# Performance work log

Measured on AMD Instinct MI355X. Metric: run time of the kernel, lower is better.

## Reference

```python
import jax, jax.numpy as jnp
import numpy as np

N = 100000
E = 1600000
F1 = 512
F3 = 128
H = 128
C = 64
SW = 0.2
FW = 1.0 - SW
BN_EPS = 1e-5


def setup_inputs() -> dict:
    key = jax.random.key(0)
    ks = jax.random.split(key, 12)
    def glorot(k, shape):
        lim = float(np.sqrt(6.0 / (shape[0] + shape[1])))
        return jax.random.uniform(k, shape, jnp.float32, -lim, lim)
    return {
        "x1": jax.random.normal(ks[0], (N, F1), jnp.float32),
        "x2": jax.random.normal(ks[1], (N, F3), jnp.float32),
        "edge_index": jax.random.randint(ks[2], (2, E), 0, N, jnp.int64),
        "W1": glorot(ks[3], (F1, H)), "b1": jnp.zeros((H,), jnp.float32),
        "W2": glorot(ks[4], (F3, H)), "b2": jnp.zeros((H,), jnp.float32),
        "Wg1": glorot(ks[5], (H, H)), "bg1": jnp.zeros((H,), jnp.float32),
        "Wg2": glorot(ks[6], (H, C)), "bg2": jnp.zeros((C,), jnp.float32),
        "gamma": jnp.ones((H,), jnp.float32), "beta": jnp.zeros((H,), jnp.float32),
        "rmean": jnp.zeros((H,), jnp.float32), "rvar": jnp.ones((H,), jnp.float32),
    }


def reference(x1, x2, edge_index, W1, b1, W2, b2, Wg1, bg1, Wg2, bg2, gamma, beta, rmean, rvar):
    # Embedding blend: fw * lin1(features) + sw * lin2(structural embedding)
    h = FW * (x1 @ W1 + b1) + SW * (x2 @ W2 + b2)  # [N, H]
    src, dst = edge_index[0], edge_index[1]
    # GCNConv layer 1 (normalize=False, add_self_loops=False): transform then scatter-add
    z = h @ Wg1                                              # [N, H]
    agg = jax.ops.segment_sum(z[src], dst, num_segments=N) + bg1  # [N, H]
    # BatchNorm1d (eval, running stats) + ReLU; dropout is identity in eval
    agg = (agg - rmean) * jax.lax.rsqrt(rvar + BN_EPS) * gamma + beta
    agg = jax.nn.relu(agg)
    # GCNConv layer 2 -> logits
    z2 = agg @ Wg2                                           # [N, C]
    out = jax.ops.segment_sum(z2[src], dst, num_segments=N) + bg2
    return out
```

## Files before the change

### kernel.cpp

```cpp
#include <hip/hip_runtime.h>
#include <hip/hip_fp16.h>
#include <cstddef>

#define NN    100000
#define EE    1600000
#define F1D   512
#define F3D   128
#define HD    128
#define CD    64
#define SWc   0.2f
#define FWc   0.8f
#define BN_EPS 1e-5f

#define SCAN_B 1024
#define NB ((NN + SCAN_B - 1) / SCAN_B)

#define BSH   7
#define NBKA  1024
#define NBUK  ((NN + 127) / 128)
#define CHK   4096
#define BCAP  8192

typedef _Float16 half8 __attribute__((ext_vector_type(8)));
typedef float f32x4 __attribute__((ext_vector_type(4)));

__global__ __launch_bounds__(256) void count_kernel(
    const int* __restrict__ dst, int* __restrict__ deg)
{
    int e = blockIdx.x * 256 + threadIdx.x;
    if (e < EE) atomicAdd(&deg[dst[e]], 1);
}

__global__ __launch_bounds__(SCAN_B) void scan_partial_kernel(
    const int* __restrict__ deg, int* __restrict__ partials)
{
    __shared__ int sh[SCAN_B / 64];
    int i = blockIdx.x * SCAN_B + threadIdx.x;
    int v = (i < NN) ? deg[i] : 0;
#pragma unroll
    for (int d = 32; d > 0; d >>= 1) v += __shfl_down(v, d, 64);
    int lane = threadIdx.x & 63, wv = threadIdx.x >> 6;
    if (lane == 0) sh[wv] = v;
    __syncthreads();
    if (threadIdx.x < SCAN_B / 64) {
        int s = sh[threadIdx.x];
#pragma unroll
        for (int d = SCAN_B / 128; d > 0; d >>= 1) s += __shfl_down(s, d, 64);
        if (threadIdx.x == 0) partials[blockIdx.x] = s;
    }
}

__global__ __launch_bounds__(128) void scan_base_kernel(
    int* __restrict__ partials, int* __restrict__ offsets)
{
    __shared__ int sh[128];
    int t = threadIdx.x;
    int v = (t < NB) ? partials[t] : 0;
    sh[t] = v;
    __syncthreads();
    for (int d = 1; d < 128; d <<= 1) {
        int u = (t >= d) ? sh[t - d] : 0;
        __syncthreads();
        sh[t] += u;
        __syncthreads();
    }
    if (t < NB) partials[t] = sh[t] - v;
    if (t == NB - 1) offsets[NN] = sh[t];
}

__global__ __launch_bounds__(SCAN_B) void scan_apply_kernel(
    const int* __restrict__ deg, const int* __restrict__ partials,
    int* __restrict__ offsets, int* __restrict__ cursor)
{
    __shared__ int sh[SCAN_B];
    int t = threadIdx.x;
    int i = blockIdx.x * SCAN_B + t;
    int v = (i < NN) ? deg[i] : 0;
    sh[t] = v;
    __syncthreads();
    for (int d = 1; d < SCAN_B; d <<= 1) {
        int u = (t >= d) ? sh[t - d] : 0;
        __syncthreads();
        sh[t] += u;
        __syncthreads();
    }
    if (i < NN) {
        int excl = sh[t] - v + partials[blockIdx.x];
        offsets[i] = excl;
        cursor[i]  = excl;
    }
}

__global__ __launch_bounds__(256) void binit_kernel(
    const int* __restrict__ offsets, int* __restrict__ gcur)
{
    int b = blockIdx.x * 256 + threadIdx.x;
    if (b < NBKA) {
        int n = b << BSH;
        if (n > NN) n = NN;
        gcur[b] = offsets[n];
    }
}

__global__ __launch_bounds__(256) void bucket_kernel(
    const int* __restrict__ src, const int* __restrict__ dst,
    int* __restrict__ gcur, int* __restrict__ ebuf)
{
    __shared__ int hist[NBKA];
    __shared__ int gb2[NBKA];
    __shared__ int tsum[256];
    __shared__ int stage[CHK];
    __shared__ int destg[CHK];

    const int t  = threadIdx.x;
    const int e0 = blockIdx.x * CHK;
    int ecnt = EE - e0;
    if (ecnt > CHK) ecnt = CHK;

    for (int b = t; b < NBKA; b += 256) hist[b] = 0;
    __syncthreads();

    for (int i = t; i < ecnt; i += 256) {
        int d = dst[e0 + i];
        atomicAdd(&hist[d >> BSH], 1);
    }
    __syncthreads();

    int a0 = hist[4 * t], a1 = hist[4 * t + 1];
    int a2 = hist[4 * t + 2], a3 = hist[4 * t + 3];
    int tot = a0 + a1 + a2 + a3;
    tsum[t] = tot;
    __syncthreads();
    for (int d = 1; d < 256; d <<= 1) {
        int u = (t >= d) ? tsum[t - d] : 0;
        __syncthreads();
        tsum[t] += u;
        __syncthreads();
    }
    int base = tsum[t] - tot;
    int o0 = base, o1 = base + a0, o2 = base + a0 + a1, o3 = base + a0 + a1 + a2;
    if (a0 > 0) gb2[4 * t]     = atomicAdd(&gcur[4 * t],     a0) - o0;
    if (a1 > 0) gb2[4 * t + 1] = atomicAdd(&gcur[4 * t + 1], a1) - o1;
    if (a2 > 0) gb2[4 * t + 2] = atomicAdd(&gcur[4 * t + 2], a2) - o2;
    if (a3 > 0) gb2[4 * t + 3] = atomicAdd(&gcur[4 * t + 3], a3) - o3;
    hist[4 * t] = o0; hist[4 * t + 1] = o1;
    hist[4 * t + 2] = o2; hist[4 * t + 3] = o3;
    __syncthreads();

    for (int i = t; i < ecnt; i += 256) {
        int d = dst[e0 + i];
        int s = src[e0 + i];
        int b = d >> BSH;
        int pos = atomicAdd(&hist[b], 1);
        stage[pos] = (s << BSH) | (d & 127);
        destg[pos] = gb2[b] + pos;
    }
    __syncthreads();

    for (int sx = t; sx < ecnt; sx += 256) ebuf[destg[sx]] = stage[sx];
}

__global__ __launch_bounds__(256) void csr_place_kernel(
    const int* __restrict__ ebuf, const int* __restrict__ offsets,
    int* __restrict__ cursor, int* __restrict__ csr)
{
    __shared__ int lcur[128];
    __shared__ int stage[BCAP];

    const int b   = blockIdx.x;
    const int t   = threadIdx.x;
    const int nb0 = b << BSH;
    int nb1 = nb0 + 128;
    if (nb1 > NN) nb1 = NN;
    const int rbeg = offsets[nb0];
    const int rend = offsets[nb1];
    const int L = rend - rbeg;

    if (L <= BCAP) {
        if (t < nb1 - nb0) lcur[t] = offsets[nb0 + t] - rbeg;
        __syncthreads();
        for (int e = rbeg + t; e < rend; e += 256) {
            int p = ebuf[e];
            int pos = atomicAdd(&lcur[p & 127], 1);
            stage[pos] = p >> BSH;
        }
        __syncthreads();
        for (int s = t; s < L; s += 256) csr[rbeg + s] = stage[s];
    } else {
        for (int e = rbeg + t; e < rend; e += 256) {
            int p = ebuf[e];
            int node = nb0 + (p & 127);
            int pos = atomicAdd(&cursor[node], 1);
            csr[pos] = p >> BSH;
        }
    }
}

__global__ __launch_bounds__(256) void prep_kernel(
    const float* __restrict__ W1, const float* __restrict__ W2,
    const float* __restrict__ Wg1, const float* __restrict__ Wg2,
    const float* __restrict__ b1, const float* __restrict__ b2,
    _Float16* __restrict__ Wc_t, _Float16* __restrict__ Wg1_t,
    _Float16* __restrict__ Wg2_t, float* __restrict__ hbuf)
{
    int i = blockIdx.x * 256 + threadIdx.x;
    if (i < 128 * 640) {
        int n = i / 640, k = i % 640;
        float v = (k < F1D) ? FWc * W1[(size_t)k * HD + n]
                            : SWc * W2[(size_t)(k - F1D) * HD + n];
        Wc_t[i] = (_Float16)v;
    } else if (i < 128 * 640 + 128 * 128) {
        int j = i - 128 * 640; int n = j / 128, k = j % 128;
        Wg1_t[j] = (_Float16)Wg1[(size_t)k * HD + n];
    } else if (i < 128 * 640 + 128 * 128 + 64 * 128) {
        int j = i - 128 * 640 - 128 * 128; int n = j / 128, k = j % 128;
        Wg2_t[j] = (_Float16)Wg2[(size_t)k * CD + n];
    } else if (i < 128 * 640 + 128 * 128 + 64 * 128 + 128) {
        int j = i - (128 * 640 + 128 * 128 + 64 * 128);
        hbuf[j] = FWc * b1[j] + SWc * b2[j];
    }
}

__global__ __launch_bounds__(256) void gemm1_mfma(
    const float* __restrict__ x1, const float* __restrict__ x2,
    const _Float16* __restrict__ Wc_t, const _Float16* __restrict__ Wg1_t,
    const float* __restrict__ hbuf, _Float16* __restrict__ z)
{
    __shared__ __align__(16) _Float16 As[128][72];
    __shared__ __align__(16) _Float16 Bs[128][72];
    __shared__ __align__(16) _Float16 Hs[128][136];

    const int tid  = threadIdx.x;
    const int wave = tid >> 6;
    const int lane = tid & 63;
    const int quad = lane >> 4;
    const int l16  = lane & 15;
    const int row0 = blockIdx.x * 128;

    const int sr = tid >> 1;
    const int sc = (tid & 1) * 32;

    f32x4 acc[2][8];
    const f32x4 zero4 = {0.f, 0.f, 0.f, 0.f};
#pragma unroll
    for (int mi = 0; mi < 2; ++mi)
#pragma unroll
        for (int ni = 0; ni < 8; ++ni) acc[mi][ni] = zero4;

    for (int t = 0; t < 10; ++t) {
        const float* xp; int stride, kb;
        if (t < 8) { xp = x1; stride = F1D; kb = t * 64; }
        else       { xp = x2; stride = F3D; kb = (t - 8) * 64; }
        __syncthreads();
        {
            int gr = row0 + sr;
            if (gr < NN) {
                const float4* rp = (const float4*)(xp + (size_t)gr * stride + kb + sc);
#pragma unroll
                for (int i = 0; i < 4; ++i) {
                    float4 f0 = rp[2 * i];
                    float4 f1 = rp[2 * i + 1];
                    half8 hv = { (_Float16)f0.x, (_Float16)f0.y, (_Float16)f0.z, (_Float16)f0.w,
                                 (_Float16)f1.x, (_Float16)f1.y, (_Float16)f1.z, (_Float16)f1.w };
                    *(half8*)&As[sr][sc + i * 8] = hv;
                }
            } else {
                half8 zv = { (_Float16)0.f, (_Float16)0.f, (_Float16)0.f, (_Float16)0.f,
                             (_Float16)0.f, (_Float16)0.f, (_Float16)0.f, (_Float16)0.f };
#pragma unroll
                for (int i = 0; i < 4; ++i) *(half8*)&As[sr][sc + i * 8] = zv;
            }
            const _Float16* wp = Wc_t + (size_t)sr * 640 + t * 64 + sc;
#pragma unroll
            for (int i = 0; i < 4; ++i)
                *(half8*)&Bs[sr][sc + i * 8] = *(const half8*)(wp + i * 8);
        }
        __syncthreads();
#pragma unroll
        for (int ks = 0; ks < 2; ++ks) {
            half8 a[2], b[8];
#pragma unroll
            for (int mi = 0; mi < 2; ++mi)
                a[mi] = *(const half8*)&As[wave * 32 + mi * 16 + l16][ks * 32 + quad * 8];
#pragma unroll
            for (int ni = 0; ni < 8; ++ni)
                b[ni] = *(const half8*)&Bs[ni * 16 + l16][ks * 32 + quad * 8];
#pragma unroll
            for (int mi = 0; mi < 2; ++mi)
#pragma unroll
                for (int ni = 0; ni < 8; ++ni)
                    acc[mi][ni] = __builtin_amdgcn_mfma_f32_16x16x32_f16(
                        a[mi], b[ni], acc[mi][ni], 0, 0, 0);
        }
    }

    {
        float hbv[8];
#pragma unroll
        for (int ni = 0; ni < 8; ++ni) hbv[ni] = hbuf[ni * 16 + l16];
#pragma unroll
        for (int mi = 0; mi < 2; ++mi)
#pragma unroll
            for (int ni = 0; ni < 8; ++ni)
#pragma unroll
                for (int r = 0; r < 4; ++r)
                    Hs[wave * 32 + mi * 16 + quad * 4 + r][ni * 16 + l16] =
                        (_Float16)(acc[mi][ni][r] + hbv[ni]);
    }

#pragma unroll
    for (int mi = 0; mi < 2; ++mi)
#pragma unroll
        for (int ni = 0; ni < 8; ++ni) acc[mi][ni] = zero4;

    for (int t = 0; t < 2; ++t) {
        __syncthreads();
        {
            const _Float16* wp = Wg1_t + (size_t)sr * 128 + t * 64 + sc;
#pragma unroll
            for (int i = 0; i < 4; ++i)
                *(half8*)&Bs[sr][sc + i * 8] = *(const half8*)(wp + i * 8);
        }
        __syncthreads();
#pragma unroll
        for (int ks = 0; ks < 2; ++ks) {
            half8 a[2], b[8];
#pragma unroll
            for (int mi = 0; mi < 2; ++mi)
                a[mi] = *(const half8*)&Hs[wave * 32 + mi * 16 + l16][t * 64 + ks * 32 + quad * 8];
#pragma unroll
            for (int ni = 0; ni < 8; ++ni)
                b[ni] = *(const half8*)&Bs[ni * 16 + l16][ks * 32 + quad * 8];
#pragma unroll
            for (int mi = 0; mi < 2; ++mi)
#pragma unroll
                for (int ni = 0; ni < 8; ++ni)
                    acc[mi][ni] = __builtin_amdgcn_mfma_f32_16x16x32_f16(
                        a[mi], b[ni], acc[mi][ni], 0, 0, 0);
        }
    }

#pragma unroll
    for (int mi = 0; mi < 2; ++mi)
#pragma unroll
        for (int ni = 0; ni < 8; ++ni)
#pragma unroll
            for (int r = 0; r < 4; ++r)
                Hs[wave * 32 + mi * 16 + quad * 4 + r][ni * 16 + l16] =
                    (_Float16)acc[mi][ni][r];
    __syncthreads();
    {
        int gr = row0 + sr;
        if (gr < NN) {
            int c0 = (tid & 1) * 64;
            _Float16* zp = z + (size_t)gr * HD + c0;
#pragma unroll
            for (int i = 0; i < 8; ++i)
                *(half8*)(zp + i * 8) = *(const half8*)&Hs[sr][c0 + i * 8];
        }
    }
}

__global__ __launch_bounds__(256) void gemm2_mfma(
    const float* __restrict__ agg, const _Float16* __restrict__ Wg2_t,
    const float* __restrict__ bg1, const float* __restrict__ gamma,
    const float* __restrict__ beta, const float* __restrict__ rmean,
    const float* __restrict__ rvar, _Float16* __restrict__ z2)
{
    __shared__ __align__(16) _Float16 As[128][72];
    __shared__ __align__(16) _Float16 Bs[64][72];
    __shared__ float sS[HD], sT[HD];

    const int tid = threadIdx.x;
    if (tid < HD) {
        float s = gamma[tid] * rsqrtf(rvar[tid] + BN_EPS);
        sS[tid] = s;
        sT[tid] = (bg1[tid] - rmean[tid]) * s + beta[tid];
    }
    __syncthreads();

    const int wave = tid >> 6;
    const int lane = tid & 63;
    const int quad = lane >> 4;
    const int l16  = lane & 15;
    const int row0 = blockIdx.x * 128;
    const int sr = tid >> 1;
    const int sc = (tid & 1) * 32;

    f32x4 acc[2][4];
    const f32x4 zero4 = {0.f, 0.f, 0.f, 0.f};
#pragma unroll
    for (int mi = 0; mi < 2; ++mi)
#pragma unroll
        for (int ni = 0; ni < 4; ++ni) acc[mi][ni] = zero4;

    for (int t = 0; t < 2; ++t) {
        __syncthreads();
        {
            int gr = row0 + sr;
            if (gr < NN) {
                const float4* rp = (const float4*)(agg + (size_t)gr * HD + t * 64 + sc);
#pragma unroll
                for (int i = 0; i < 4; ++i) {
                    float4 f0 = rp[2 * i];
                    float4 f1 = rp[2 * i + 1];
                    int k = t * 64 + sc + i * 8;
                    float v0 = fmaxf(fmaf(f0.x, sS[k + 0], sT[k + 0]), 0.f);
                    float v1 = fmaxf(fmaf(f0.y, sS[k + 1], sT[k + 1]), 0.f);
                    float v2 = fmaxf(fmaf(f0.z, sS[k + 2], sT[k + 2]), 0.f);
                    float v3 = fmaxf(fmaf(f0.w, sS[k + 3], sT[k + 3]), 0.f);
                    float v4 = fmaxf(fmaf(f1.x, sS[k + 4], sT[k + 4]), 0.f);
                    float v5 = fmaxf(fmaf(f1.y, sS[k + 5], sT[k + 5]), 0.f);
                    float v6 = fmaxf(fmaf(f1.z, sS[k + 6], sT[k + 6]), 0.f);
                    float v7 = fmaxf(fmaf(f1.w, sS[k + 7], sT[k + 7]), 0.f);
                    half8 hv = { (_Float16)v0, (_Float16)v1, (_Float16)v2, (_Float16)v3,
                                 (_Float16)v4, (_Float16)v5, (_Float16)v6, (_Float16)v7 };
                    *(half8*)&As[sr][sc + i * 8] = hv;
                }
            } else {
                half8 zv = { (_Float16)0.f, (_Float16)0.f, (_Float16)0.f, (_Float16)0.f,
                             (_Float16)0.f, (_Float16)0.f, (_Float16)0.f, (_Float16)0.f };
#pragma unroll
                for (int i = 0; i < 4; ++i) *(half8*)&As[sr][sc + i * 8] = zv;
            }
            int n = tid >> 2, c = (tid & 3) * 16;
            const _Float16* wp = Wg2_t + (size_t)n * 128 + t * 64 + c;
            *(half8*)&Bs[n][c]     = *(const half8*)wp;
            *(half8*)&Bs[n][c + 8] = *(const half8*)(wp + 8);
        }
        __syncthreads();
#pragma unroll
        for (int ks = 0; ks < 2; ++ks) {
            half8 a[2], b[4];
#pragma unroll
            for (int mi = 0; mi < 2; ++mi)
                a[mi] = *(const half8*)&As[wave * 32 + mi * 16 + l16][ks * 32 + quad * 8];
#pragma unroll
            for (int ni = 0; ni < 4; ++ni)
                b[ni] = *(const half8*)&Bs[ni * 16 + l16][ks * 32 + quad * 8];
#pragma unroll
            for (int mi = 0; mi < 2; ++mi)
#pragma unroll
                for (int ni = 0; ni < 4; ++ni)
                    acc[mi][ni] = __builtin_amdgcn_mfma_f32_16x16x32_f16(
                        a[mi], b[ni], acc[mi][ni], 0, 0, 0);
        }
    }

    __syncthreads();
#pragma unroll
    for (int mi = 0; mi < 2; ++mi)
#pragma unroll
        for (int ni = 0; ni < 4; ++ni)
#pragma unroll
            for (int r = 0; r < 4; ++r)
                As[wave * 32 + mi * 16 + quad * 4 + r][ni * 16 + l16] =
                    (_Float16)acc[mi][ni][r];
    __syncthreads();
    {
        int gr = row0 + sr;
        if (gr < NN) {
            _Float16* zp = z2 + (size_t)gr * CD + sc;
            *(half8*)(zp)      = *(const half8*)&As[sr][sc];
            *(half8*)(zp + 8)  = *(const half8*)&As[sr][sc + 8];
            *(half8*)(zp + 16) = *(const half8*)&As[sr][sc + 16];
            *(half8*)(zp + 24) = *(const half8*)&As[sr][sc + 24];
        }
    }
}

__global__ __launch_bounds__(256) void gather1_kernel(
    const _Float16* __restrict__ z, const int* __restrict__ offsets,
    const int* __restrict__ csr_src, float* __restrict__ agg)
{
    int node = blockIdx.x * 4 + (threadIdx.x >> 6);
    if (node >= NN) return;
    const int lane = threadIdx.x & 63;
    const int h  = lane >> 4;
    const int fl = lane & 15;

    int beg = offsets[node];
    int cnt = offsets[node + 1] - beg;

    float a0 = 0.f, a1 = 0.f, a2 = 0.f, a3 = 0.f;
    float a4 = 0.f, a5 = 0.f, a6 = 0.f, a7 = 0.f;

    for (int j0 = 0; j0 < cnt; j0 += 64) {
        int cntc = cnt - j0; if (cntc > 64) cntc = 64;
        int myidx = (lane < cntc) ? csr_src[beg + j0 + lane] : 0;
        int nq = (cntc + 3) >> 2;
#pragma unroll 4
        for (int i = 0; i < nq; ++i) {
            int e = i * 4 + h;
            int si = __shfl(myidx, e);
            float m = (e < cntc) ? 1.f : 0.f;
            float4 raw = *(const float4*)(z + (size_t)si * HD + fl * 8);
            const __half2* hp = (const __half2*)&raw;
            float2 f0 = __half22float2(hp[0]);
            float2 f1 = __half22float2(hp[1]);
            float2 f2 = __half22float2(hp[2]);
            float2 f3 = __half22float2(hp[3]);
            a0 = fmaf(m, f0.x, a0); a1 = fmaf(m, f0.y, a1);
            a2 = fmaf(m, f1.x, a2); a3 = fmaf(m, f1.y, a3);
            a4 = fmaf(m, f2.x, a4); a5 = fmaf(m, f2.y, a5);
            a6 = fmaf(m, f3.x, a6); a7 = fmaf(m, f3.y, a7);
        }
    }

    a0 += __shfl_xor(a0, 16); a1 += __shfl_xor(a1, 16);
    a2 += __shfl_xor(a2, 16); a3 += __shfl_xor(a3, 16);
    a4 += __shfl_xor(a4, 16); a5 += __shfl_xor(a5, 16);
    a6 += __shfl_xor(a6, 16); a7 += __shfl_xor(a7, 16);
    a0 += __shfl_xor(a0, 32); a1 += __shfl_xor(a1, 32);
    a2 += __shfl_xor(a2, 32); a3 += __shfl_xor(a3, 32);
    a4 += __shfl_xor(a4, 32); a5 += __shfl_xor(a5, 32);
    a6 += __shfl_xor(a6, 32); a7 += __shfl_xor(a7, 32);

    if (h == 0) {
        float* op = agg + (size_t)node * HD + fl * 8;
        float4 o0 = make_float4(a0, a1, a2, a3);
        float4 o1 = make_float4(a4, a5, a6, a7);
        *(float4*)op       = o0;
        *(float4*)(op + 4) = o1;
    }
}

__global__ __launch_bounds__(256) void gather2_kernel(
    const _Float16* __restrict__ z2, const int* __restrict__ offsets,
    const int* __restrict__ csr_src, const float* __restrict__ bg2,
    float* __restrict__ out)
{
    int node = blockIdx.x * 4 + (threadIdx.x >> 6);
    if (node >= NN) return;
    const int lane = threadIdx.x & 63;
    const int h  = lane >> 4;
    const int fl = lane & 15;

    int beg = offsets[node];
    int cnt = offsets[node + 1] - beg;

    float a0 = 0.f, a1 = 0.f, a2 = 0.f, a3 = 0.f;

    for (int j0 = 0; j0 < cnt; j0 += 64) {
        int cntc = cnt - j0; if (cntc > 64) cntc = 64;
        int myidx = (lane < cntc) ? csr_src[beg + j0 + lane] : 0;
        int nq = (cntc + 3) >> 2;
#pragma unroll 4
        for (int i = 0; i < nq; ++i) {
            int e = i * 4 + h;
            int si = __shfl(myidx, e);
            float m = (e < cntc) ? 1.f : 0.f;
            float2 raw = *(const float2*)(z2 + (size_t)si * CD + fl * 4);
            const __half2* hp = (const __half2*)&raw;
            float2 f0 = __half22float2(hp[0]);
            float2 f1 = __half22float2(hp[1]);
            a0 = fmaf(m, f0.x, a0); a1 = fmaf(m, f0.y, a1);
            a2 = fmaf(m, f1.x, a2); a3 = fmaf(m, f1.y, a3);
        }
    }

    a0 += __shfl_xor(a0, 16); a1 += __shfl_xor(a1, 16);
    a2 += __shfl_xor(a2, 16); a3 += __shfl_xor(a3, 16);
    a0 += __shfl_xor(a0, 32); a1 += __shfl_xor(a1, 32);
    a2 += __shfl_xor(a2, 32); a3 += __shfl_xor(a3, 32);

    if (h == 0) {
        float4 bv = *(const float4*)(bg2 + fl * 4);
        float4 o = make_float4(a0 + bv.x, a1 + bv.y, a2 + bv.z, a3 + bv.w);
        *(float4*)(out + (size_t)node * CD + fl * 4) = o;
    }
}

extern "C" void kernel_launch(void* const* d_in, const int* in_sizes, int n_in,
                              void* d_out, int out_size, void* d_ws, size_t ws_size,
                              hipStream_t stream)
{
    const float* x1    = (const float*)d_in[0];
    const float* x2    = (const float*)d_in[1];
    const int*   ei    = (const int*)d_in[2];
    const float* W1    = (const float*)d_in[3];
    const float* b1    = (const float*)d_in[4];
    const float* W2    = (const float*)d_in[5];
    const float* b2    = (const float*)d_in[6];
    const float* Wg1   = (const float*)d_in[7];
    const float* bg1   = (const float*)d_in[8];
    const float* Wg2   = (const float*)d_in[9];
    const float* bg2   = (const float*)d_in[10];
    const float* gamma = (const float*)d_in[11];
    const float* beta  = (const float*)d_in[12];
    const float* rmean = (const float*)d_in[13];
    const float* rvar  = (const float*)d_in[14];
    float* out = (float*)d_out;

    char* p = (char*)d_ws;
    _Float16* z_h  = (_Float16*)p; p += (size_t)NN * HD * sizeof(_Float16);
    float*  agg    = (float*)p;    p += (size_t)NN * HD * sizeof(float);
    int*    csr    = (int*)p;      p += (size_t)EE * sizeof(int);
    int*    offs   = (int*)p;      p += (size_t)(NN + 16) * sizeof(int);
    int*    curs   = (int*)p;      p += (size_t)(NN + 16) * sizeof(int);
    int*    deg    = (int*)p;      p += (size_t)(NN + 16) * sizeof(int);
    int*    parts  = (int*)p;      p += (size_t)(NB + 16) * sizeof(int);
    int*    gcur   = (int*)p;      p += (size_t)(NBKA + 16) * sizeof(int);
    _Float16* Wc_t = (_Float16*)p; p += (size_t)128 * 640 * sizeof(_Float16);
    _Float16* Wg1t = (_Float16*)p; p += (size_t)128 * 128 * sizeof(_Float16);
    _Float16* Wg2t = (_Float16*)p; p += (size_t)64 * 128 * sizeof(_Float16);
    float*  hbuf   = (float*)p;    p += 128 * sizeof(float);
    _Float16* z2_h = z_h;
    int*    ebuf   = (int*)agg;

    const int* src = ei;
    const int* dst = ei + EE;

    prep_kernel<<<(128 * 640 + 128 * 128 + 64 * 128 + 128 + 255) / 256, 256, 0, stream>>>(
        W1, W2, Wg1, Wg2, b1, b2, Wc_t, Wg1t, Wg2t, hbuf);

    hipMemsetAsync(deg, 0, (size_t)NN * sizeof(int), stream);
    count_kernel<<<(EE + 255) / 256, 256, 0, stream>>>(dst, deg);
    scan_partial_kernel<<<NB, SCAN_B, 0, stream>>>(deg, parts);
    scan_base_kernel<<<1, 128, 0, stream>>>(parts, offs);
    scan_apply_kernel<<<NB, SCAN_B, 0, stream>>>(deg, parts, offs, curs);
    binit_kernel<<<(NBKA + 255) / 256, 256, 0, stream>>>(offs, gcur);
    bucket_kernel<<<(EE + CHK - 1) / CHK, 256, 0, stream>>>(src, dst, gcur, ebuf);
    csr_place_kernel<<<NBUK, 256, 0, stream>>>(ebuf, offs, curs, csr);

    gemm1_mfma<<<(NN + 127) / 128, 256, 0, stream>>>(x1, x2, Wc_t, Wg1t, hbuf, z_h);
    gather1_kernel<<<(NN + 3) / 4, 256, 0, stream>>>(z_h, offs, csr, agg);
    gemm2_mfma<<<(NN + 127) / 128, 256, 0, stream>>>(agg, Wg2t, bg1, gamma, beta,
                                                     rmean, rvar, z2_h);
    gather2_kernel<<<(NN + 3) / 4, 256, 0, stream>>>(z2_h, offs, csr, bg2, out);
}
```

Measured before the change: 641.2 us.

## Prefetch next gemm1 K-tile into registers and alias LDS buffers for occupancy

gemm1 now loads the next K-tile of x and the fused weights into registers while MFMAs run on the current LDS tile, so global load latency overlaps with compute. The LDS arrays are packed into one dynamic pool in which Hs aliases As/Bs, and the second GEMM gets its own Bs2 region. Launch bounds request 3 blocks per CU. The register prefetch raises VGPR pressure, and the occupancy hint may force spills.

```diff
diff --git a/kernel.cpp b/kernel.cpp
--- a/kernel.cpp
+++ b/kernel.cpp
@@ -20,6 +20,8 @@
 #define NBUK  ((NN + 127) / 128)
 #define CHK   4096
 #define BCAP  8192
+
+#define G1_LDS 53248
 
 typedef _Float16 half8 __attribute__((ext_vector_type(8)));
 typedef float f32x4 __attribute__((ext_vector_type(4)));
@@ -221,14 +223,16 @@
     }
 }
 
-__global__ __launch_bounds__(256) void gemm1_mfma(
+__global__ __launch_bounds__(256, 3) void gemm1_mfma(
     const float* __restrict__ x1, const float* __restrict__ x2,
     const _Float16* __restrict__ Wc_t, const _Float16* __restrict__ Wg1_t,
     const float* __restrict__ hbuf, _Float16* __restrict__ z)
 {
-    __shared__ __align__(16) _Float16 As[128][72];
-    __shared__ __align__(16) _Float16 Bs[128][72];
-    __shared__ __align__(16) _Float16 Hs[128][136];
+    extern __shared__ char pool[];
+    _Float16 (*As)[72]  = (_Float16(*)[72])pool;
+    _Float16 (*Bs)[72]  = (_Float16(*)[72])(pool + 18432);
+    _Float16 (*Hs)[136] = (_Float16(*)[136])pool;
+    _Float16 (*Bs2)[72] = (_Float16(*)[72])(pool + 34816);
 
     const int tid  = threadIdx.x;
     const int wave = tid >> 6;
@@ -239,6 +243,8 @@
 
     const int sr = tid >> 1;
     const int sc = (tid & 1) * 32;
+    const int gr = row0 + sr;
+    const bool valid = gr < NN;
 
     f32x4 acc[2][8];
     const f32x4 zero4 = {0.f, 0.f, 0.f, 0.f};
@@ -247,35 +253,56 @@
 #pragma unroll
         for (int ni = 0; ni < 8; ++ni) acc[mi][ni] = zero4;
 
+    float4 xr[8];
+    half8  wr[4];
+
+    {
+        if (valid) {
+            const float4* rp = (const float4*)(x1 + (size_t)gr * F1D + sc);
+#pragma unroll
+            for (int i = 0; i < 8; ++i) xr[i] = rp[i];
+        }
+        const _Float16* wp = Wc_t + (size_t)sr * 640 + sc;
+#pragma unroll
+        for (int i = 0; i < 4; ++i) wr[i] = *(const half8*)(wp + i * 8);
+    }
+
     for (int t = 0; t < 10; ++t) {
-        const float* xp; int stride, kb;
-        if (t < 8) { xp = x1; stride = F1D; kb = t * 64; }
-        else       { xp = x2; stride = F3D; kb = (t - 8) * 64; }
-        __syncthreads();
-        {
-            int gr = row0 + sr;
-            if (gr < NN) {
+        if (valid) {
+#pragma unroll
+            for (int i = 0; i < 4; ++i) {
+                float4 f0 = xr[2 * i];
+                float4 f1 = xr[2 * i + 1];
+                half8 hv = { (_Float16)f0.x, (_Float16)f0.y, (_Float16)f0.z, (_Float16)f0.w,
+                             (_Float16)f1.x, (_Float16)f1.y, (_Float16)f1.z, (_Float16)f1.w };
+                *(half8*)&As[sr][sc + i * 8] = hv;
+            }
+        } else {
+            half8 zv = { (_Float16)0.f, (_Float16)0.f, (_Float16)0.f, (_Float16)0.f,
+                         (_Float16)0.f, (_Float16)0.f, (_Float16)0.f, (_Float16)0.f };
+#pragma unroll
+            for (int i = 0; i < 4; ++i) *(half8*)&As[sr][sc + i * 8] = zv;
+        }
+#pragma unroll
+        for (int i = 0; i < 4; ++i)
+            *(half8*)&Bs[sr][sc + i * 8] = wr[i];
+
+        __syncthreads();
+
+        if (t + 1 < 10) {
+            const float* xp; int stride, kb;
+            if (t + 1 < 8) { xp = x1; stride = F1D; kb = (t + 1) * 64; }
+            else           { xp = x2; stride = F3D; kb = (t + 1 - 8) * 64; }
+            if (valid) {
                 const float4* rp = (const float4*)(xp + (size_t)gr * stride + kb + sc);
 #pragma unroll
-                for (int i = 0; i < 4; ++i) {
-                    float4 f0 = rp[2 * i];
-                    float4 f1 = rp[2 * i + 1];
-                    half8 hv = { (_Float16)f0.x, (_Float16)f0.y, (_Float16)f0.z, (_Float16)f0.w,
-                                 (_Float16)f1.x, (_Float16)f1.y, (_Float16)f1.z, (_Float16)f1.w };
-                    *(half8*)&As[sr][sc + i * 8] = hv;
-                }
-            } else {
-                half8 zv = { (_Float16)0.f, (_Float16)0.f, (_Float16)0.f, (_Float16)0.f,
-                             (_Float16)0.f, (_Float16)0.f, (_Float16)0.f, (_Float16)0.f };
-#pragma unroll
-                for (int i = 0; i < 4; ++i) *(half8*)&As[sr][sc + i * 8] = zv;
+                for (int i = 0; i < 8; ++i) xr[i] = rp[i];
             }
-            const _Float16* wp = Wc_t + (size_t)sr * 640 + t * 64 + sc;
-#pragma unroll
-            for (int i = 0; i < 4; ++i)
-                *(half8*)&Bs[sr][sc + i * 8] = *(const half8*)(wp + i * 8);
-        }
-        __syncthreads();
+            const _Float16* wp = Wc_t + (size_t)sr * 640 + (t + 1) * 64 + sc;
+#pragma unroll
+            for (int i = 0; i < 4; ++i) wr[i] = *(const half8*)(wp + i * 8);
+        }
+
 #pragma unroll
         for (int ks = 0; ks < 2; ++ks) {
             half8 a[2], b[8];
@@ -292,6 +319,7 @@
                     acc[mi][ni] = __builtin_amdgcn_mfma_f32_16x16x32_f16(
                         a[mi], b[ni], acc[mi][ni], 0, 0, 0);
         }
+        __syncthreads();
     }
 
     {
@@ -319,7 +347,7 @@
             const _Float16* wp = Wg1_t + (size_t)sr * 128 + t * 64 + sc;
 #pragma unroll
             for (int i = 0; i < 4; ++i)
-                *(half8*)&Bs[sr][sc + i * 8] = *(const half8*)(wp + i * 8);
+                *(half8*)&Bs2[sr][sc + i * 8] = *(const half8*)(wp + i * 8);
         }
         __syncthreads();
 #pragma unroll
@@ -330,7 +358,7 @@
                 a[mi] = *(const half8*)&Hs[wave * 32 + mi * 16 + l16][t * 64 + ks * 32 + quad * 8];
 #pragma unroll
             for (int ni = 0; ni < 8; ++ni)
-                b[ni] = *(const half8*)&Bs[ni * 16 + l16][ks * 32 + quad * 8];
+                b[ni] = *(const half8*)&Bs2[ni * 16 + l16][ks * 32 + quad * 8];
 #pragma unroll
             for (int mi = 0; mi < 2; ++mi)
 #pragma unroll
@@ -350,8 +378,7 @@
                     (_Float16)acc[mi][ni][r];
     __syncthreads();
     {
-        int gr = row0 + sr;
-        if (gr < NN) {
+        if (valid) {
             int c0 = (tid & 1) * 64;
             _Float16* zp = z + (size_t)gr * HD + c0;
 #pragma unroll
@@ -623,7 +650,7 @@
     bucket_kernel<<<(EE + CHK - 1) / CHK, 256, 0, stream>>>(src, dst, gcur, ebuf);
     csr_place_kernel<<<NBUK, 256, 0, stream>>>(ebuf, offs, curs, csr);
 
-    gemm1_mfma<<<(NN + 127) / 128, 256, 0, stream>>>(x1, x2, Wc_t, Wg1t, hbuf, z_h);
+    gemm1_mfma<<<(NN + 127) / 128, 256, G1_LDS, stream>>>(x1, x2, Wc_t, Wg1t, hbuf, z_h);
     gather1_kernel<<<(NN + 3) / 4, 256, 0, stream>>>(z_h, offs, csr, agg);
     gemm2_mfma<<<(NN + 127) / 128, 256, 0, stream>>>(agg, Wg2t, bg1, gamma, beta,
                                                      rmean, rvar, z2_h);
```

New measurement: 638.4 us. About the same (-0.4%).

## Fold Wg1 into the blended embedding weights and retile gemm1

Applied to the files above, without the earlier changes.

A new prep kernel precomputes the fused weight (FW*W1 ; SW*W2) @ Wg1 and the fused bias, so gemm1 runs a single 640x128 GEMM instead of a GEMM followed by a second 128x128 GEMM and an intermediate fp16 store of h. gemm1 now uses 64-row tiles with larger K chunks (256) and fewer barriers, and reads B fragments straight from global/L2 instead of staging them in LDS. It also sets launch bounds for 4 blocks per CU. The costs are that B loads are no longer shared through LDS, and the fused product is rounded to fp16 once, which changes numerics slightly.

```diff
diff --git a/kernel.cpp b/kernel.cpp
--- a/kernel.cpp
+++ b/kernel.cpp
@@ -197,166 +197,151 @@
 }
 
 __global__ __launch_bounds__(256) void prep_kernel(
+    const float* __restrict__ Wg2, const float* __restrict__ b1,
+    const float* __restrict__ b2, _Float16* __restrict__ Wg2_t,
+    float* __restrict__ hbuf)
+{
+    int i = blockIdx.x * 256 + threadIdx.x;
+    if (i < 64 * 128) {
+        int n = i / 128, k = i % 128;
+        Wg2_t[i] = (_Float16)Wg2[(size_t)k * CD + n];
+    } else if (i < 64 * 128 + 128) {
+        int j = i - 64 * 128;
+        hbuf[j] = FWc * b1[j] + SWc * b2[j];
+    }
+}
+
+__global__ __launch_bounds__(128) void prep_fuse_kernel(
     const float* __restrict__ W1, const float* __restrict__ W2,
-    const float* __restrict__ Wg1, const float* __restrict__ Wg2,
-    const float* __restrict__ b1, const float* __restrict__ b2,
-    _Float16* __restrict__ Wc_t, _Float16* __restrict__ Wg1_t,
-    _Float16* __restrict__ Wg2_t, float* __restrict__ hbuf)
-{
-    int i = blockIdx.x * 256 + threadIdx.x;
-    if (i < 128 * 640) {
-        int n = i / 640, k = i % 640;
-        float v = (k < F1D) ? FWc * W1[(size_t)k * HD + n]
+    const float* __restrict__ Wg1, const float* __restrict__ hbuf,
+    _Float16* __restrict__ Wf_t, float* __restrict__ bz)
+{
+    __shared__ float wrow[128];
+    const int k = blockIdx.x;
+    const int n = threadIdx.x;
+    if (k < 640) {
+        wrow[n] = (k < F1D) ? FWc * W1[(size_t)k * HD + n]
                             : SWc * W2[(size_t)(k - F1D) * HD + n];
-        Wc_t[i] = (_Float16)v;
-    } else if (i < 128 * 640 + 128 * 128) {
-        int j = i - 128 * 640; int n = j / 128, k = j % 128;
-        Wg1_t[j] = (_Float16)Wg1[(size_t)k * HD + n];
-    } else if (i < 128 * 640 + 128 * 128 + 64 * 128) {
-        int j = i - 128 * 640 - 128 * 128; int n = j / 128, k = j % 128;
-        Wg2_t[j] = (_Float16)Wg2[(size_t)k * CD + n];
-    } else if (i < 128 * 640 + 128 * 128 + 64 * 128 + 128) {
-        int j = i - (128 * 640 + 128 * 128 + 64 * 128);
-        hbuf[j] = FWc * b1[j] + SWc * b2[j];
-    }
-}
-
-__global__ __launch_bounds__(256) void gemm1_mfma(
+        __syncthreads();
+        float acc = 0.f;
+#pragma unroll 8
+        for (int j = 0; j < 128; ++j)
+            acc = fmaf(wrow[j], Wg1[(size_t)j * HD + n], acc);
+        Wf_t[(size_t)n * 640 + k] = (_Float16)acc;
+    } else {
+        wrow[n] = hbuf[n];
+        __syncthreads();
+        float acc = 0.f;
+#pragma unroll 8
+        for (int j = 0; j < 128; ++j)
+            acc = fmaf(wrow[j], Wg1[(size_t)j * HD + n], acc);
+        bz[n] = acc;
+    }
+}
+
+__global__ __launch_bounds__(256, 4) void gemm1_mfma(
     const float* __restrict__ x1, const float* __restrict__ x2,
-    const _Float16* __restrict__ Wc_t, const _Float16* __restrict__ Wg1_t,
-    const float* __restrict__ hbuf, _Float16* __restrict__ z)
-{
-    __shared__ __align__(16) _Float16 As[128][72];
-    __shared__ __align__(16) _Float16 Bs[128][72];
-    __shared__ __align__(16) _Float16 Hs[128][136];
+    const _Float16* __restrict__ Wf_t, const float* __restrict__ bz,
+    _Float16* __restrict__ z)
+{
+    __shared__ __align__(16) _Float16 As[64][264];
 
     const int tid  = threadIdx.x;
     const int wave = tid >> 6;
     const int lane = tid & 63;
     const int quad = lane >> 4;
     const int l16  = lane & 15;
-    const int row0 = blockIdx.x * 128;
-
-    const int sr = tid >> 1;
-    const int sc = (tid & 1) * 32;
-
-    f32x4 acc[2][8];
+    const int row0 = blockIdx.x * 64;
+
+    const int sr = tid >> 2;
+    const int sq = tid & 3;
+    const int gr = row0 + sr;
+    const bool valid = gr < NN;
+
+    f32x4 acc[4][2];
     const f32x4 zero4 = {0.f, 0.f, 0.f, 0.f};
 #pragma unroll
-    for (int mi = 0; mi < 2; ++mi)
-#pragma unroll
-        for (int ni = 0; ni < 8; ++ni) acc[mi][ni] = zero4;
-
-    for (int t = 0; t < 10; ++t) {
-        const float* xp; int stride, kb;
-        if (t < 8) { xp = x1; stride = F1D; kb = t * 64; }
-        else       { xp = x2; stride = F3D; kb = (t - 8) * 64; }
+    for (int mi = 0; mi < 4; ++mi)
+#pragma unroll
+        for (int ni = 0; ni < 2; ++ni) acc[mi][ni] = zero4;
+
+#pragma unroll
+    for (int s = 0; s < 3; ++s) {
+        const int kbW = s * 256;
+        const int BKs = (s < 2) ? 256 : 128;
+        const float* xp = (s < 2) ? (x1 + (size_t)gr * F1D + s * 256)
+                                  : (x2 + (size_t)gr * F3D);
+        const int scf = sq * (BKs >> 2);
         __syncthreads();
         {
-            int gr = row0 + sr;
-            if (gr < NN) {
-                const float4* rp = (const float4*)(xp + (size_t)gr * stride + kb + sc);
-#pragma unroll
-                for (int i = 0; i < 4; ++i) {
-                    float4 f0 = rp[2 * i];
-                    float4 f1 = rp[2 * i + 1];
-                    half8 hv = { (_Float16)f0.x, (_Float16)f0.y, (_Float16)f0.z, (_Float16)f0.w,
+            const int nf4 = BKs >> 4;
+            if (valid) {
+                const float4* rp = (const float4*)(xp + scf);
+#pragma unroll
+                for (int c = 0; c < nf4; c += 4) {
+                    float4 f0 = rp[c], f1 = rp[c + 1];
+                    float4 f2 = rp[c + 2], f3 = rp[c + 3];
+                    half8 h0 = { (_Float16)f0.x, (_Float16)f0.y, (_Float16)f0.z, (_Float16)f0.w,
                                  (_Float16)f1.x, (_Float16)f1.y, (_Float16)f1.z, (_Float16)f1.w };
-                    *(half8*)&As[sr][sc + i * 8] = hv;
+                    half8 h1 = { (_Float16)f2.x, (_Float16)f2.y, (_Float16)f2.z, (_Float16)f2.w,
+                                 (_Float16)f3.x, (_Float16)f3.y, (_Float16)f3.z, (_Float16)f3.w };
+                    *(half8*)&As[sr][scf + c * 4]     = h0;
+                    *(half8*)&As[sr][scf + c * 4 + 8] = h1;
                 }
             } else {
                 half8 zv = { (_Float16)0.f, (_Float16)0.f, (_Float16)0.f, (_Float16)0.f,
                              (_Float16)0.f, (_Float16)0.f, (_Float16)0.f, (_Float16)0.f };
 #pragma unroll
-                for (int i = 0; i < 4; ++i) *(half8*)&As[sr][sc + i * 8] = zv;
+                for (int c = 0; c < nf4; c += 4) {
+                    *(half8*)&As[sr][scf + c * 4]     = zv;
+                    *(half8*)&As[sr][scf + c * 4 + 8] = zv;
+                }
             }
-            const _Float16* wp = Wc_t + (size_t)sr * 640 + t * 64 + sc;
-#pragma unroll
-            for (int i = 0; i < 4; ++i)
-                *(half8*)&Bs[sr][sc + i * 8] = *(const half8*)(wp + i * 8);
-        }
-        __syncthreads();
-#pragma unroll
-        for (int ks = 0; ks < 2; ++ks) {
-            half8 a[2], b[8];
-#pragma unroll
-            for (int mi = 0; mi < 2; ++mi)
-                a[mi] = *(const half8*)&As[wave * 32 + mi * 16 + l16][ks * 32 + quad * 8];
-#pragma unroll
-            for (int ni = 0; ni < 8; ++ni)
-                b[ni] = *(const half8*)&Bs[ni * 16 + l16][ks * 32 + quad * 8];
-#pragma unroll
-            for (int mi = 0; mi < 2; ++mi)
-#pragma unroll
-                for (int ni = 0; ni < 8; ++ni)
+        }
+        __syncthreads();
+
+        const int nks = BKs >> 5;
+        const _Float16* bbase = Wf_t + (size_t)(wave * 32 + l16) * 640 + kbW + quad * 8;
+#pragma unroll
+        for (int ks = 0; ks < nks; ++ks) {
+            half8 a[4], b[2];
+#pragma unroll
+            for (int mi = 0; mi < 4; ++mi)
+                a[mi] = *(const half8*)&As[mi * 16 + l16][ks * 32 + quad * 8];
+            b[0] = *(const half8*)(bbase + ks * 32);
+            b[1] = *(const half8*)(bbase + 16 * 640 + ks * 32);
+#pragma unroll
+            for (int mi = 0; mi < 4; ++mi)
+#pragma unroll
+                for (int ni = 0; ni < 2; ++ni)
                     acc[mi][ni] = __builtin_amdgcn_mfma_f32_16x16x32_f16(
                         a[mi], b[ni], acc[mi][ni], 0, 0, 0);
         }
     }
 
+    __syncthreads();
     {
-        float hbv[8];
-#pragma unroll
-        for (int ni = 0; ni < 8; ++ni) hbv[ni] = hbuf[ni * 16 + l16];
-#pragma unroll
-        for (int mi = 0; mi < 2; ++mi)
-#pragma unroll
-            for (int ni = 0; ni < 8; ++ni)
+        float bzv[2];
+        bzv[0] = bz[wave * 32 + l16];
+        bzv[1] = bz[wave * 32 + 16 + l16];
+#pragma unroll
+        for (int mi = 0; mi < 4; ++mi)
+#pragma unroll
+            for (int ni = 0; ni < 2; ++ni)
 #pragma unroll
                 for (int r = 0; r < 4; ++r)
-                    Hs[wave * 32 + mi * 16 + quad * 4 + r][ni * 16 + l16] =
-                        (_Float16)(acc[mi][ni][r] + hbv[ni]);
-    }
-
-#pragma unroll
-    for (int mi = 0; mi < 2; ++mi)
-#pragma unroll
-        for (int ni = 0; ni < 8; ++ni) acc[mi][ni] = zero4;
-
-    for (int t = 0; t < 2; ++t) {
-        __syncthreads();
-        {
-            const _Float16* wp = Wg1_t + (size_t)sr * 128 + t * 64 + sc;
+                    As[mi * 16 + quad * 4 + r][wave * 32 + ni * 16 + l16] =
+                        (_Float16)(acc[mi][ni][r] + bzv[ni]);
+    }
+    __syncthreads();
+    {
+        int zr = tid >> 2;
+        int c0 = (tid & 3) * 32;
+        if (row0 + zr < NN) {
+            _Float16* zp = z + (size_t)(row0 + zr) * HD + c0;
 #pragma unroll
             for (int i = 0; i < 4; ++i)
-                *(half8*)&Bs[sr][sc + i * 8] = *(const half8*)(wp + i * 8);
-        }
-        __syncthreads();
-#pragma unroll
-        for (int ks = 0; ks < 2; ++ks) {
-            half8 a[2], b[8];
-#pragma unroll
-            for (int mi = 0; mi < 2; ++mi)
-                a[mi] = *(const half8*)&Hs[wave * 32 + mi * 16 + l16][t * 64 + ks * 32 + quad * 8];
-#pragma unroll
-            for (int ni = 0; ni < 8; ++ni)
-                b[ni] = *(const half8*)&Bs[ni * 16 + l16][ks * 32 + quad * 8];
-#pragma unroll
-            for (int mi = 0; mi < 2; ++mi)
-#pragma unroll
-                for (int ni = 0; ni < 8; ++ni)
-                    acc[mi][ni] = __builtin_amdgcn_mfma_f32_16x16x32_f16(
-                        a[mi], b[ni], acc[mi][ni], 0, 0, 0);
-        }
-    }
-
-#pragma unroll
-    for (int mi = 0; mi < 2; ++mi)
-#pragma unroll
-        for (int ni = 0; ni < 8; ++ni)
-#pragma unroll
-            for (int r = 0; r < 4; ++r)
-                Hs[wave * 32 + mi * 16 + quad * 4 + r][ni * 16 + l16] =
-                    (_Float16)acc[mi][ni][r];
-    __syncthreads();
-    {
-        int gr = row0 + sr;
-        if (gr < NN) {
-            int c0 = (tid & 1) * 64;
-            _Float16* zp = z + (size_t)gr * HD + c0;
-#pragma unroll
-            for (int i = 0; i < 8; ++i)
-                *(half8*)(zp + i * 8) = *(const half8*)&Hs[sr][c0 + i * 8];
+                *(half8*)(zp + i * 8) = *(const half8*)&As[zr][c0 + i * 8];
         }
     }
 }
@@ -601,9 +586,9 @@
     int*    deg    = (int*)p;      p += (size_t)(NN + 16) * sizeof(int);
     int*    parts  = (int*)p;      p += (size_t)(NB + 16) * sizeof(int);
     int*    gcur   = (int*)p;      p += (size_t)(NBKA + 16) * sizeof(int);
-    _Float16* Wc_t = (_Float16*)p; p += (size_t)128 * 640 * sizeof(_Float16);
-    _Float16* Wg1t = (_Float16*)p; p += (size_t)128 * 128 * sizeof(_Float16);
+    _Float16* Wf_t = (_Float16*)p; p += (size_t)128 * 640 * sizeof(_Float16);
     _Float16* Wg2t = (_Float16*)p; p += (size_t)64 * 128 * sizeof(_Float16);
+    float*  bz     = (float*)p;    p += 128 * sizeof(float);
     float*  hbuf   = (float*)p;    p += 128 * sizeof(float);
     _Float16* z2_h = z_h;
     int*    ebuf   = (int*)agg;
@@ -611,8 +596,9 @@
     const int* src = ei;
     const int* dst = ei + EE;
 
-    prep_kernel<<<(128 * 640 + 128 * 128 + 64 * 128 + 128 + 255) / 256, 256, 0, stream>>>(
-        W1, W2, Wg1, Wg2, b1, b2, Wc_t, Wg1t, Wg2t, hbuf);
+    prep_kernel<<<(64 * 128 + 128 + 255) / 256, 256, 0, stream>>>(
+        Wg2, b1, b2, Wg2t, hbuf);
+    prep_fuse_kernel<<<641, 128, 0, stream>>>(W1, W2, Wg1, hbuf, Wf_t, bz);
 
     hipMemsetAsync(deg, 0, (size_t)NN * sizeof(int), stream);
     count_kernel<<<(EE + 255) / 256, 256, 0, stream>>>(dst, deg);
@@ -623,7 +609,7 @@
     bucket_kernel<<<(EE + CHK - 1) / CHK, 256, 0, stream>>>(src, dst, gcur, ebuf);
     csr_place_kernel<<<NBUK, 256, 0, stream>>>(ebuf, offs, curs, csr);
 
-    gemm1_mfma<<<(NN + 127) / 128, 256, 0, stream>>>(x1, x2, Wc_t, Wg1t, hbuf, z_h);
+    gemm1_mfma<<<(NN + 63) / 64, 256, 0, stream>>>(x1, x2, Wf_t, bz, z_h);
     gather1_kernel<<<(NN + 3) / 4, 256, 0, stream>>>(z_h, offs, csr, agg);
     gemm2_mfma<<<(NN + 127) / 128, 256, 0, stream>>>(agg, Wg2t, bg1, gamma, beta,
                                                      rmean, rvar, z2_h);
```

Measured after the change: 650.4 us. No clear change (+1.4%).
